# Performance work log

Hardware: AMD Instinct MI355X
Metric: run time of the kernel (lower is better)

Reference implementation:

```python
import jax, jax.numpy as jnp
import numpy as np

B, T, H = 4, 1024, 4096
N_Q, N_KV, HD = 32, 8, 128
N_REP = N_Q // N_KV
THETA = 10000.0


def setup_inputs() -> dict:
    key = jax.random.key(0)
    k0, k1, k2 = jax.random.split(key, 3)
    x = jax.random.normal(k0, (B, T, H), dtype=jnp.float32)
    w_qkv = jax.random.normal(k1, ((N_Q + 2 * N_KV) * HD, H), dtype=jnp.float32) * 0.02
    w_proj = jax.random.normal(k2, (N_Q * HD, H), dtype=jnp.float32).T * 0.02  # [H, N_Q*HD] -> stored as [out,in]=[4096,4096]
    # real RoPE frequencies, matching precompute_freqs_cis(theta=10000)
    inv_freq = 1.0 / (THETA ** (np.arange(0, HD, 2, dtype=np.float32) / HD))  # [HD/2]
    angles = np.arange(T, dtype=np.float32)[:, None] * inv_freq[None, :]      # [T, HD/2]
    freqs_cos = jnp.asarray(np.cos(angles))
    freqs_sin = jnp.asarray(np.sin(angles))
    return {"x": x, "w_qkv": w_qkv, "w_proj": w_proj,
            "freqs_cos": freqs_cos, "freqs_sin": freqs_sin}


def _rope(x, cos, sin):
    # x: [B, T, nH, HD]; consecutive pairs (x[2i], x[2i+1]) form complex numbers
    x0 = x[..., 0::2]
    x1 = x[..., 1::2]
    c = cos[None, :, None, :]
    s = sin[None, :, None, :]
    r0 = x0 * c - x1 * s
    r1 = x0 * s + x1 * c
    return jnp.stack([r0, r1], axis=-1).reshape(x.shape)


def reference(x, w_qkv, w_proj, freqs_cos, freqs_sin):
    q_per_kv = N_Q // N_KV
    qkv = jnp.einsum('bth,oh->bto', x, w_qkv)                 # [B,T,(N_Q+2*N_KV)*HD]
    qkv = qkv.reshape(B, T, N_KV, q_per_kv + 2, HD)           # interleaved GQA layout
    q = qkv[:, :, :, :q_per_kv, :].reshape(B, T, N_Q, HD)
    k = qkv[:, :, :, q_per_kv, :]                              # [B,T,N_KV,HD]
    v = qkv[:, :, :, q_per_kv + 1, :]
    q = _rope(q, freqs_cos, freqs_sin)
    k = _rope(k, freqs_cos, freqs_sin)
    k = jnp.repeat(k, N_REP, axis=2)                           # [B,T,N_Q,HD]
    v = jnp.repeat(v, N_REP, axis=2)
    q = q.transpose(0, 2, 1, 3)                                # [B,H,T,HD]
    k = k.transpose(0, 2, 1, 3)
    v = v.transpose(0, 2, 1, 3)
    scale = 1.0 / jnp.sqrt(jnp.float32(HD))
    scores = jnp.einsum('bhqd,bhkd->bhqk', q, k) * scale       # [B,H,T,T]
    causal = jnp.tril(jnp.ones((T, T), dtype=bool))
    scores = jnp.where(causal[None, None], scores, jnp.finfo(scores.dtype).min)
    attn = jax.nn.softmax(scores, axis=-1)
    out = jnp.einsum('bhqk,bhkd->bhqd', attn, v)               # [B,H,T,HD]
    out = out.transpose(0, 2, 1, 3).reshape(B, T, N_Q * HD)
    return jnp.einsum('bto,ho->bth', out, w_proj)              # RowParallel proj, [B,T,H]
```

## Files before the change

### kernel.cpp

```cpp
#include <hip/hip_runtime.h>
#include <cstddef>

#define DEVINL __device__ __forceinline__

typedef float f32x4 __attribute__((ext_vector_type(4)));
typedef __bf16 bf16x8 __attribute__((ext_vector_type(8)));

DEVINL unsigned short f2bf(float f) {
  union { float f; unsigned int u; } v; v.f = f;
  unsigned int u = v.u;
  unsigned int r = (u + 0x7fffu + ((u >> 16) & 1u)) >> 16;
  return (unsigned short)r;
}
DEVINL float bf2f(unsigned short s) {
  union { unsigned int u; float f; } v; v.u = ((unsigned int)s) << 16;
  return v.f;
}
DEVINL uint4 pack8(const unsigned short o[8]) {
  uint4 r;
  r.x = (unsigned int)o[0] | ((unsigned int)o[1] << 16);
  r.y = (unsigned int)o[2] | ((unsigned int)o[3] << 16);
  r.z = (unsigned int)o[4] | ((unsigned int)o[5] << 16);
  r.w = (unsigned int)o[6] | ((unsigned int)o[7] << 16);
  return r;
}
DEVINL void gload16(const void* g, void* l) {
  __builtin_amdgcn_global_load_lds(
      (__attribute__((address_space(1))) void*)g,
      (__attribute__((address_space(3))) void*)l, 16, 0, 0);
}

__global__ __launch_bounds__(256) void k_cvt(const float* __restrict__ in,
                                             unsigned short* __restrict__ out, int n4) {
  int i = blockIdx.x * 256 + threadIdx.x;
  if (i >= n4) return;
  float4 v = ((const float4*)in)[i];
  ushort4 o;
  o.x = f2bf(v.x); o.y = f2bf(v.y); o.z = f2bf(v.z); o.w = f2bf(v.w);
  ((ushort4*)out)[i] = o;
}

template <int OUT_BF16>
__global__ __launch_bounds__(512, 1) void k_gemm256(const unsigned short* __restrict__ A,
                                                    const unsigned short* __restrict__ Bt,
                                                    void* __restrict__ Cout,
                                                    int M, int N, int K) {
  __shared__ __align__(16) unsigned short As[2][2][256 * 32];
  __shared__ __align__(16) unsigned short Bs[2][2][256 * 32];
  const int t = threadIdx.x, lane = t & 63;
  const int wid = t >> 6, wm = wid >> 2, wn = wid & 3;
  const int fr = lane & 15, kq = lane >> 4;
  const int nwg = gridDim.x * gridDim.y;
  int lin = blockIdx.y * gridDim.x + blockIdx.x;
  lin = (lin & 7) * (nwg >> 3) + (lin >> 3);
  const int bx = lin % gridDim.x, by = lin / gridDim.x;
  const int row0 = by * 256, col0 = bx * 256;
  const int NT = K >> 6;

  int srow[2], sgs[2];
#pragma unroll
  for (int i = 0; i < 2; ++i) {
    const int off = (i * 512 + t) * 16;
    srow[i] = off >> 6;
    sgs[i] = (((off >> 4) & 3) - (srow[i] >> 1)) & 3;
  }

#define STAGE_A(KT, KS)                                                        \
  do {                                                                         \
    const int b_ = (KT) & 1;                                                   \
    _Pragma("unroll") for (int i = 0; i < 2; ++i)                              \
        gload16(A + (size_t)(row0 + srow[i]) * K + (KT) * 64 + (KS) * 32 +     \
                    sgs[i] * 8,                                                \
                (char*)&As[b_][KS][0] + i * 8192 + wid * 1024);                \
  } while (0)
#define STAGE_B(KT, KS)                                                        \
  do {                                                                         \
    const int b_ = (KT) & 1;                                                   \
    _Pragma("unroll") for (int i = 0; i < 2; ++i)                              \
        gload16(Bt + (size_t)(col0 + srow[i]) * K + (KT) * 64 + (KS) * 32 +    \
                    sgs[i] * 8,                                                \
                (char*)&Bs[b_][KS][0] + i * 8192 + wid * 1024);                \
  } while (0)
#define LDFRAG(BUFP, ROW) \
  (*(const bf16x8*)((const char*)(BUFP) + (ROW) * 64 + ((((ROW) >> 1) + kq & 3) << 4)))

  f32x4 acc[8][4];
#pragma unroll
  for (int m = 0; m < 8; ++m)
#pragma unroll
    for (int n = 0; n < 4; ++n) acc[m][n] = f32x4{0.f, 0.f, 0.f, 0.f};

  STAGE_A(0, 0); STAGE_B(0, 0); STAGE_A(0, 1); STAGE_B(0, 1);
  STAGE_A(1, 0); STAGE_B(1, 0);
  asm volatile("s_waitcnt vmcnt(4)" ::: "memory");
  __builtin_amdgcn_s_barrier();

  for (int kt = 0; kt < NT; ++kt) {
    const unsigned short* As0 = &As[kt & 1][0][0];
    const unsigned short* As1 = &As[kt & 1][1][0];
    const unsigned short* Bs0 = &Bs[kt & 1][0][0];
    const unsigned short* Bs1 = &Bs[kt & 1][1][0];
    bf16x8 a0[4], a1[4], b0[4], b1[4];

#pragma unroll
    for (int m = 0; m < 4; ++m) a0[m] = LDFRAG(As0, wm * 128 + m * 16 + fr);
#pragma unroll
    for (int n = 0; n < 4; ++n) b0[n] = LDFRAG(Bs0, wn * 64 + n * 16 + fr);
    if (kt + 1 < NT) STAGE_A(kt + 1, 1);
    __builtin_amdgcn_sched_barrier(0);
    __builtin_amdgcn_s_barrier();
    asm volatile("s_waitcnt lgkmcnt(0)" ::: "memory");
    __builtin_amdgcn_sched_barrier(0);
    __builtin_amdgcn_s_setprio(1);
#pragma unroll
    for (int m = 0; m < 4; ++m)
#pragma unroll
      for (int n = 0; n < 4; ++n)
        acc[m][n] = __builtin_amdgcn_mfma_f32_16x16x32_bf16(a0[m], b0[n], acc[m][n], 0, 0, 0);
    __builtin_amdgcn_s_setprio(0);
    __builtin_amdgcn_s_barrier();

#pragma unroll
    for (int m = 0; m < 4; ++m) a1[m] = LDFRAG(As0, wm * 128 + 64 + m * 16 + fr);
    if (kt + 1 < NT) STAGE_B(kt + 1, 1);
    __builtin_amdgcn_sched_barrier(0);
    __builtin_amdgcn_s_barrier();
    asm volatile("s_waitcnt lgkmcnt(0)" ::: "memory");
    __builtin_amdgcn_sched_barrier(0);
    __builtin_amdgcn_s_setprio(1);
#pragma unroll
    for (int m = 0; m < 4; ++m)
#pragma unroll
      for (int n = 0; n < 4; ++n)
        acc[m + 4][n] = __builtin_amdgcn_mfma_f32_16x16x32_bf16(a1[m], b0[n], acc[m + 4][n], 0, 0, 0);
    __builtin_amdgcn_s_setprio(0);
    __builtin_amdgcn_s_barrier();

#pragma unroll
    for (int m = 0; m < 4; ++m) a0[m] = LDFRAG(As1, wm * 128 + m * 16 + fr);
#pragma unroll
    for (int n = 0; n < 4; ++n) b1[n] = LDFRAG(Bs1, wn * 64 + n * 16 + fr);
    if (kt + 2 < NT) STAGE_A(kt + 2, 0);
    __builtin_amdgcn_sched_barrier(0);
    __builtin_amdgcn_s_barrier();
    asm volatile("s_waitcnt lgkmcnt(0)" ::: "memory");
    __builtin_amdgcn_sched_barrier(0);
    __builtin_amdgcn_s_setprio(1);
#pragma unroll
    for (int m = 0; m < 4; ++m)
#pragma unroll
      for (int n = 0; n < 4; ++n)
        acc[m][n] = __builtin_amdgcn_mfma_f32_16x16x32_bf16(a0[m], b1[n], acc[m][n], 0, 0, 0);
    __builtin_amdgcn_s_setprio(0);
    __builtin_amdgcn_s_barrier();

#pragma unroll
    for (int m = 0; m < 4; ++m) a1[m] = LDFRAG(As1, wm * 128 + 64 + m * 16 + fr);
    if (kt + 1 < NT) {
      if (kt + 2 < NT) asm volatile("s_waitcnt vmcnt(2)" ::: "memory");
      else             asm volatile("s_waitcnt vmcnt(0)" ::: "memory");
    }
    if (kt + 2 < NT) STAGE_B(kt + 2, 0);
    __builtin_amdgcn_sched_barrier(0);
    __builtin_amdgcn_s_barrier();
    asm volatile("s_waitcnt lgkmcnt(0)" ::: "memory");
    __builtin_amdgcn_sched_barrier(0);
    __builtin_amdgcn_s_setprio(1);
#pragma unroll
    for (int m = 0; m < 4; ++m)
#pragma unroll
      for (int n = 0; n < 4; ++n)
        acc[m + 4][n] = __builtin_amdgcn_mfma_f32_16x16x32_bf16(a1[m], b1[n], acc[m + 4][n], 0, 0, 0);
    __builtin_amdgcn_s_setprio(0);
    __builtin_amdgcn_s_barrier();
  }
#undef STAGE_A
#undef STAGE_B
#undef LDFRAG

  const int rsub = kq * 4;
#pragma unroll
  for (int m = 0; m < 8; ++m)
#pragma unroll
    for (int n = 0; n < 4; ++n)
#pragma unroll
      for (int r = 0; r < 4; ++r) {
        const size_t row = (size_t)row0 + wm * 128 + m * 16 + rsub + r;
        const size_t col = (size_t)col0 + wn * 64 + n * 16 + fr;
        if (OUT_BF16)
          ((unsigned short*)Cout)[row * N + col] = f2bf(acc[m][n][r]);
        else
          ((float*)Cout)[row * N + col] = acc[m][n][r];
      }
}

__global__ __launch_bounds__(256) void k_rope(const unsigned short* __restrict__ qkv,
                                              const float* __restrict__ fcos,
                                              const float* __restrict__ fsin,
                                              unsigned short* __restrict__ Qb,
                                              unsigned short* __restrict__ Kb) {
  const int idx = blockIdx.x * 256 + threadIdx.x;
  if (idx >= 4096 * 640) return;
  const int bt = idx / 640;
  const int r = idx - bt * 640;
  const int g = r / 80;
  const int rr = r - g * 80;
  const int slot = rr >> 4;
  const int d0 = (rr & 15) * 8;
  const int o0 = g * 768 + slot * 128 + d0;
  const int b = bt >> 10, tt = bt & 1023;

  uint4 raw = *(const uint4*)&qkv[(size_t)bt * 6144 + o0];
  unsigned short us[8] = {
      (unsigned short)(raw.x & 0xffff), (unsigned short)(raw.x >> 16),
      (unsigned short)(raw.y & 0xffff), (unsigned short)(raw.y >> 16),
      (unsigned short)(raw.z & 0xffff), (unsigned short)(raw.z >> 16),
      (unsigned short)(raw.w & 0xffff), (unsigned short)(raw.w >> 16)};

  float4 c = *(const float4*)&fcos[tt * 64 + (d0 >> 1)];
  float4 s = *(const float4*)&fsin[tt * 64 + (d0 >> 1)];
  const float sc = (slot < 4) ? 0.08838834764831845f : 1.0f;
  float cj[4] = {c.x, c.y, c.z, c.w};
  float sj[4] = {s.x, s.y, s.z, s.w};
  unsigned short os[8];
#pragma unroll
  for (int j = 0; j < 4; ++j) {
    float x0 = bf2f(us[2 * j]), x1 = bf2f(us[2 * j + 1]);
    os[2 * j] = f2bf((x0 * cj[j] - x1 * sj[j]) * sc);
    os[2 * j + 1] = f2bf((x0 * sj[j] + x1 * cj[j]) * sc);
  }
  if (slot < 4) {
    const int h = g * 4 + slot;
    *(uint4*)&Qb[((size_t)(b * 32 + h) * 1024 + tt) * 128 + d0] = pack8(os);
  } else {
    *(uint4*)&Kb[((size_t)(b * 8 + g) * 1024 + tt) * 128 + d0] = pack8(os);
  }
}

__global__ __launch_bounds__(256) void k_vtrans(const unsigned short* __restrict__ qkv,
                                                unsigned short* __restrict__ VT) {
  const int t = threadIdx.x;
  const int tt0 = blockIdx.x * 128;
  const int bg = blockIdx.y;
  const int b = bg >> 3, g = bg & 7;
  const int tj = t & 15;
  const int ti = t >> 4;
  union U4 { uint4 v; unsigned int u[4]; };
  U4 in[8], out[8];
  const unsigned short* src =
      qkv + (size_t)(b * 1024 + tt0 + ti * 8) * 6144 + g * 768 + 640 + tj * 8;
#pragma unroll
  for (int r = 0; r < 8; ++r) in[r].v = *(const uint4*)(src + (size_t)r * 6144);
#pragma unroll
  for (int c = 0; c < 8; ++c) {
    const unsigned int sel = (c & 1) ? 0x07060302u : 0x05040100u;
    const int dw = c >> 1;
#pragma unroll
    for (int w = 0; w < 4; ++w)
      out[c].u[w] = __builtin_amdgcn_perm(in[2 * w + 1].u[dw], in[2 * w].u[dw], sel);
  }
  unsigned short* dst = VT + (size_t)bg * 131072 + (size_t)(tj * 8) * 1024 + tt0 + ti * 8;
#pragma unroll
  for (int c = 0; c < 8; ++c) *(uint4*)(dst + (size_t)c * 1024) = out[c].v;
}

__global__ __launch_bounds__(512, 1) void k_attn(const unsigned short* __restrict__ Qb,
                                                 const unsigned short* __restrict__ Kb,
                                                 const unsigned short* __restrict__ VT,
                                                 unsigned short* __restrict__ AO) {
  __shared__ __align__(16) unsigned short Ks[2][64 * 128];
  __shared__ __align__(16) unsigned short Vt[2][128 * 64];
  __shared__ __align__(16) unsigned short Ps[8][32 * 64];
  const int t = threadIdx.x, lane = t & 63, wid = t >> 6;
  const int hh = wid >> 1, qh = wid & 1;
  const int bg = blockIdx.x, b = bg >> 3, g = bg & 7;
  const int qi = 15 - (int)blockIdx.y;
  const int q0 = qi * 64;
  const int h = g * 4 + hh;
  const int fr = lane & 15, kq = lane >> 4;
  const size_t kvbase = (size_t)bg * (1024 * 128);
  const size_t vtbase = (size_t)bg * (128 * 1024);

#define ASTAGE(TILE, BUF)                                                      \
  do {                                                                         \
    const int kv0_ = (TILE) * 64;                                              \
    _Pragma("unroll") for (int it = 0; it < 2; ++it) {                         \
      const int off = it * 8192 + t * 16;                                      \
      const int r_ = off >> 8, cb_ = off & 255;                                \
      const int scb_ = cb_ ^ ((r_ & 7) << 4);                                  \
      gload16(Kb + kvbase + (size_t)(kv0_ + r_) * 128 + (scb_ >> 1),           \
              (char*)Ks[BUF] + off);                                           \
    }                                                                          \
    _Pragma("unroll") for (int it = 0; it < 2; ++it) {                         \
      const int off = it * 8192 + t * 16;                                      \
      const int rd_ = off >> 7, cb_ = off & 127;                               \
      const int scb_ = cb_ ^ ((rd_ & 7) << 4);                                 \
      gload16(VT + vtbase + (size_t)rd_ * 1024 + kv0_ + (scb_ >> 1),           \
              (char*)Vt[BUF] + off);                                           \
    }                                                                          \
  } while (0)

  bf16x8 qf[2][4];
  {
    const unsigned short* Qp0 = Qb + ((size_t)(b * 32 + h) * 1024 + q0 + qh * 32) * 128;
#pragma unroll
    for (int qr = 0; qr < 2; ++qr)
#pragma unroll
      for (int ks = 0; ks < 4; ++ks)
        qf[qr][ks] = *(const bf16x8*)&Qp0[(size_t)(qr * 16 + fr) * 128 + ks * 32 + kq * 8];
  }
  float mrow[2][4], lrow[2][4];
#pragma unroll
  for (int qr = 0; qr < 2; ++qr)
#pragma unroll
    for (int rg = 0; rg < 4; ++rg) { mrow[qr][rg] = -1e30f; lrow[qr][rg] = 0.f; }
  f32x4 of[2][8];
#pragma unroll
  for (int qr = 0; qr < 2; ++qr)
#pragma unroll
    for (int n = 0; n < 8; ++n) of[qr][n] = f32x4{0.f, 0.f, 0.f, 0.f};

  const int ntiles = qi + 1;
  ASTAGE(0, 0);

  for (int kt = 0; kt < ntiles; ++kt) {
    const int buf = kt & 1;
    const int kv0 = kt * 64;
    if (kt + 1 < ntiles) {
      ASTAGE(kt + 1, buf ^ 1);
      asm volatile("s_waitcnt vmcnt(4)" ::: "memory");
    } else {
      asm volatile("s_waitcnt vmcnt(0)" ::: "memory");
    }
    __builtin_amdgcn_s_barrier();
    __builtin_amdgcn_sched_barrier(0);

    f32x4 sacc[2][4];
#pragma unroll
    for (int qr = 0; qr < 2; ++qr)
#pragma unroll
      for (int n = 0; n < 4; ++n) sacc[qr][n] = f32x4{0.f, 0.f, 0.f, 0.f};
#pragma unroll
    for (int n = 0; n < 4; ++n) {
      const int row = n * 16 + fr;
      const int sw = (row & 7) << 4;
      bf16x8 kf[4];
#pragma unroll
      for (int ks = 0; ks < 4; ++ks)
        kf[ks] = *(const bf16x8*)((const char*)Ks[buf] + row * 256 + ((ks * 64 + kq * 16) ^ sw));
      __builtin_amdgcn_s_setprio(1);
#pragma unroll
      for (int qr = 0; qr < 2; ++qr)
#pragma unroll
        for (int ks = 0; ks < 4; ++ks)
          sacc[qr][n] =
              __builtin_amdgcn_mfma_f32_16x16x32_bf16(qf[qr][ks], kf[ks], sacc[qr][n], 0, 0, 0);
      __builtin_amdgcn_s_setprio(0);
    }

#pragma unroll
    for (int qr = 0; qr < 2; ++qr)
#pragma unroll
      for (int rg = 0; rg < 4; ++rg) {
        const int qrow = q0 + qh * 32 + qr * 16 + kq * 4 + rg;
        float s[4];
#pragma unroll
        for (int n = 0; n < 4; ++n) {
          s[n] = sacc[qr][n][rg];
          if (kv0 + n * 16 + fr > qrow) s[n] = -1e30f;
        }
        float mx = fmaxf(fmaxf(s[0], s[1]), fmaxf(s[2], s[3]));
#pragma unroll
        for (int o = 1; o < 16; o <<= 1) mx = fmaxf(mx, __shfl_xor(mx, o));
        if (mx > mrow[qr][rg] + 8.f) {
          const float fac = __expf(mrow[qr][rg] - mx);
          lrow[qr][rg] *= fac;
#pragma unroll
          for (int n = 0; n < 8; ++n) of[qr][n][rg] *= fac;
          mrow[qr][rg] = mx;
        }
        const float mcur = mrow[qr][rg];
        float p[4];
#pragma unroll
        for (int n = 0; n < 4; ++n) p[n] = __expf(s[n] - mcur);
        float sum = (p[0] + p[1]) + (p[2] + p[3]);
#pragma unroll
        for (int o = 1; o < 16; o <<= 1) sum += __shfl_xor(sum, o);
        lrow[qr][rg] += sum;
        const int q = qr * 16 + kq * 4 + rg;
        const int swp = (q & 7) << 4;
#pragma unroll
        for (int n = 0; n < 4; ++n)
          *(unsigned short*)((char*)Ps[wid] + q * 128 + ((2 * (n * 16 + fr)) ^ swp)) =
              f2bf(p[n]);
      }
    asm volatile("s_waitcnt lgkmcnt(0)" ::: "memory");
    __builtin_amdgcn_sched_barrier(0);

    bf16x8 pa[2][2];
#pragma unroll
    for (int qr = 0; qr < 2; ++qr) {
      const int prow = qr * 16 + fr;
      const int swp = (prow & 7) << 4;
#pragma unroll
      for (int kk = 0; kk < 2; ++kk)
        pa[qr][kk] = *(const bf16x8*)((const char*)Ps[wid] + prow * 128 +
                                      ((kk * 64 + kq * 16) ^ swp));
    }
#pragma unroll
    for (int n = 0; n < 8; ++n) {
      const int row = n * 16 + fr;
      const int sw = (row & 7) << 4;
      bf16x8 vf[2];
#pragma unroll
      for (int kk = 0; kk < 2; ++kk)
        vf[kk] = *(const bf16x8*)((const char*)Vt[buf] + row * 128 + ((kk * 64 + kq * 16) ^ sw));
      __builtin_amdgcn_s_setprio(1);
#pragma unroll
      for (int qr = 0; qr < 2; ++qr)
#pragma unroll
        for (int kk = 0; kk < 2; ++kk)
          of[qr][n] = __builtin_amdgcn_mfma_f32_16x16x32_bf16(pa[qr][kk], vf[kk], of[qr][n], 0, 0, 0);
      __builtin_amdgcn_s_setprio(0);
    }
    asm volatile("s_waitcnt lgkmcnt(0)" ::: "memory");
    __builtin_amdgcn_sched_barrier(0);
    __builtin_amdgcn_s_barrier();
  }
#undef ASTAGE

  float inv[2][4];
#pragma unroll
  for (int qr = 0; qr < 2; ++qr)
#pragma unroll
    for (int rg = 0; rg < 4; ++rg) inv[qr][rg] = 1.0f / lrow[qr][rg];
#pragma unroll
  for (int qr = 0; qr < 2; ++qr)
#pragma unroll
    for (int n = 0; n < 8; ++n)
#pragma unroll
      for (int rg = 0; rg < 4; ++rg) {
        const size_t row = (size_t)b * 1024 + q0 + qh * 32 + qr * 16 + kq * 4 + rg;
        const size_t col = (size_t)h * 128 + n * 16 + fr;
        AO[row * 4096 + col] = f2bf(of[qr][n][rg] * inv[qr][rg]);
      }
}

extern "C" void kernel_launch(void* const* d_in, const int* in_sizes, int n_in,
                              void* d_out, int out_size, void* d_ws, size_t ws_size,
                              hipStream_t stream) {
  const float* x = (const float*)d_in[0];
  const float* w_qkv = (const float*)d_in[1];
  const float* w_proj = (const float*)d_in[2];
  const float* fcos = (const float*)d_in[3];
  const float* fsin = (const float*)d_in[4];
  float* out = (float*)d_out;

  char* ws = (char*)d_ws;
  unsigned short* XB    = (unsigned short*)(ws + 0);
  unsigned short* WQKVB = (unsigned short*)(ws + 33554432);
  unsigned short* QKVB  = (unsigned short*)(ws + 83886080);
  unsigned short* QB    = (unsigned short*)(ws + 134217728);
  unsigned short* KB    = (unsigned short*)(ws + 167772160);
  unsigned short* VTB   = (unsigned short*)(ws + 176160768);
  unsigned short* WPROJB = XB;
  unsigned short* AOB    = QKVB;

  k_cvt<<<16384, 256, 0, stream>>>(x, XB, 4194304);
  k_cvt<<<24576, 256, 0, stream>>>(w_qkv, WQKVB, 6291456);
  k_gemm256<1><<<dim3(24, 16), 512, 0, stream>>>(XB, WQKVB, QKVB, 4096, 6144, 4096);
  k_cvt<<<16384, 256, 0, stream>>>(w_proj, WPROJB, 4194304);
  k_rope<<<10240, 256, 0, stream>>>(QKVB, fcos, fsin, QB, KB);
  k_vtrans<<<dim3(8, 32), 256, 0, stream>>>(QKVB, VTB);
  k_attn<<<dim3(32, 16), 512, 0, stream>>>(QB, KB, VTB, AOB);
  k_gemm256<0><<<dim3(16, 16), 512, 0, stream>>>(AOB, WPROJB, out, 4096, 4096, 4096);
}
```

Before: 515.6 us.

## Switch GEMM to 32x32x16 MFMA tiles and merge conversion kernels

```diff
diff --git a/kernel.cpp b/kernel.cpp
--- a/kernel.cpp
+++ b/kernel.cpp
@@ -4,6 +4,7 @@
 #define DEVINL __device__ __forceinline__
 
 typedef float f32x4 __attribute__((ext_vector_type(4)));
+typedef float f32x16 __attribute__((ext_vector_type(16)));
 typedef __bf16 bf16x8 __attribute__((ext_vector_type(8)));
 
 DEVINL unsigned short f2bf(float f) {
@@ -30,10 +31,22 @@
       (__attribute__((address_space(3))) void*)l, 16, 0, 0);
 }
 
-__global__ __launch_bounds__(256) void k_cvt(const float* __restrict__ in,
-                                             unsigned short* __restrict__ out, int n4) {
+__global__ __launch_bounds__(256) void k_cvt_all(const float* __restrict__ x,
+                                                 const float* __restrict__ wq,
+                                                 const float* __restrict__ wp,
+                                                 unsigned short* __restrict__ xb,
+                                                 unsigned short* __restrict__ wqb,
+                                                 unsigned short* __restrict__ wpb) {
   int i = blockIdx.x * 256 + threadIdx.x;
-  if (i >= n4) return;
+  const float* in;
+  unsigned short* out;
+  if (i < 4194304) {
+    in = x; out = xb;
+  } else if (i < 4194304 + 6291456) {
+    in = wq; out = wqb; i -= 4194304;
+  } else {
+    in = wp; out = wpb; i -= 4194304 + 6291456;
+  }
   float4 v = ((const float4*)in)[i];
   ushort4 o;
   o.x = f2bf(v.x); o.y = f2bf(v.y); o.z = f2bf(v.z); o.w = f2bf(v.w);
@@ -49,7 +62,8 @@
   __shared__ __align__(16) unsigned short Bs[2][2][256 * 32];
   const int t = threadIdx.x, lane = t & 63;
   const int wid = t >> 6, wm = wid >> 2, wn = wid & 3;
-  const int fr = lane & 15, kq = lane >> 4;
+  const int lrow = lane & 31;
+  const int khalf = lane >> 5;
   const int nwg = gridDim.x * gridDim.y;
   int lin = blockIdx.y * gridDim.x + blockIdx.x;
   lin = (lin & 7) * (nwg >> 3) + (lin >> 3);
@@ -81,14 +95,17 @@
                     sgs[i] * 8,                                                \
                 (char*)&Bs[b_][KS][0] + i * 8192 + wid * 1024);                \
   } while (0)
-#define LDFRAG(BUFP, ROW) \
-  (*(const bf16x8*)((const char*)(BUFP) + (ROW) * 64 + ((((ROW) >> 1) + kq & 3) << 4)))
-
-  f32x4 acc[8][4];
-#pragma unroll
-  for (int m = 0; m < 8; ++m)
-#pragma unroll
-    for (int n = 0; n < 4; ++n) acc[m][n] = f32x4{0.f, 0.f, 0.f, 0.f};
+#define LDF32(BUFP, ROW, KK)                                                   \
+  (*(const bf16x8*)((const char*)(BUFP) + (ROW) * 64 +                         \
+                    ((((KK) * 2 + khalf + ((ROW) >> 1)) & 3) << 4)))
+
+  f32x16 acc[4][2];
+#pragma unroll
+  for (int m = 0; m < 4; ++m)
+#pragma unroll
+    for (int n = 0; n < 2; ++n)
+#pragma unroll
+      for (int r = 0; r < 16; ++r) acc[m][n][r] = 0.f;
 
   STAGE_A(0, 0); STAGE_B(0, 0); STAGE_A(0, 1); STAGE_B(0, 1);
   STAGE_A(1, 0); STAGE_B(1, 0);
@@ -100,12 +117,18 @@
     const unsigned short* As1 = &As[kt & 1][1][0];
     const unsigned short* Bs0 = &Bs[kt & 1][0][0];
     const unsigned short* Bs1 = &Bs[kt & 1][1][0];
-    bf16x8 a0[4], a1[4], b0[4], b1[4];
-
-#pragma unroll
-    for (int m = 0; m < 4; ++m) a0[m] = LDFRAG(As0, wm * 128 + m * 16 + fr);
-#pragma unroll
-    for (int n = 0; n < 4; ++n) b0[n] = LDFRAG(Bs0, wn * 64 + n * 16 + fr);
+    bf16x8 a[2][2], bfr[2][2];
+
+#pragma unroll
+    for (int m = 0; m < 2; ++m)
+#pragma unroll
+      for (int kk = 0; kk < 2; ++kk)
+        a[m][kk] = LDF32(As0, wm * 128 + m * 32 + lrow, kk);
+#pragma unroll
+    for (int n = 0; n < 2; ++n)
+#pragma unroll
+      for (int kk = 0; kk < 2; ++kk)
+        bfr[n][kk] = LDF32(Bs0, wn * 64 + n * 32 + lrow, kk);
     if (kt + 1 < NT) STAGE_A(kt + 1, 1);
     __builtin_amdgcn_sched_barrier(0);
     __builtin_amdgcn_s_barrier();
@@ -113,15 +136,21 @@
     __builtin_amdgcn_sched_barrier(0);
     __builtin_amdgcn_s_setprio(1);
 #pragma unroll
-    for (int m = 0; m < 4; ++m)
-#pragma unroll
-      for (int n = 0; n < 4; ++n)
-        acc[m][n] = __builtin_amdgcn_mfma_f32_16x16x32_bf16(a0[m], b0[n], acc[m][n], 0, 0, 0);
+    for (int m = 0; m < 2; ++m)
+#pragma unroll
+      for (int n = 0; n < 2; ++n)
+#pragma unroll
+        for (int kk = 0; kk < 2; ++kk)
+          acc[m][n] = __builtin_amdgcn_mfma_f32_32x32x16_bf16(a[m][kk], bfr[n][kk],
+                                                              acc[m][n], 0, 0, 0);
     __builtin_amdgcn_s_setprio(0);
     __builtin_amdgcn_s_barrier();
 
 #pragma unroll
-    for (int m = 0; m < 4; ++m) a1[m] = LDFRAG(As0, wm * 128 + 64 + m * 16 + fr);
+    for (int m = 0; m < 2; ++m)
+#pragma unroll
+      for (int kk = 0; kk < 2; ++kk)
+        a[m][kk] = LDF32(As0, wm * 128 + (m + 2) * 32 + lrow, kk);
     if (kt + 1 < NT) STAGE_B(kt + 1, 1);
     __builtin_amdgcn_sched_barrier(0);
     __builtin_amdgcn_s_barrier();
@@ -129,17 +158,26 @@
     __builtin_amdgcn_sched_barrier(0);
     __builtin_amdgcn_s_setprio(1);
 #pragma unroll
-    for (int m = 0; m < 4; ++m)
-#pragma unroll
-      for (int n = 0; n < 4; ++n)
-        acc[m + 4][n] = __builtin_amdgcn_mfma_f32_16x16x32_bf16(a1[m], b0[n], acc[m + 4][n], 0, 0, 0);
+    for (int m = 0; m < 2; ++m)
+#pragma unroll
+      for (int n = 0; n < 2; ++n)
+#pragma unroll
+        for (int kk = 0; kk < 2; ++kk)
+          acc[m + 2][n] = __builtin_amdgcn_mfma_f32_32x32x16_bf16(a[m][kk], bfr[n][kk],
+                                                                  acc[m + 2][n], 0, 0, 0);
     __builtin_amdgcn_s_setprio(0);
     __builtin_amdgcn_s_barrier();
 
 #pragma unroll
-    for (int m = 0; m < 4; ++m) a0[m] = LDFRAG(As1, wm * 128 + m * 16 + fr);
-#pragma unroll
-    for (int n = 0; n < 4; ++n) b1[n] = LDFRAG(Bs1, wn * 64 + n * 16 + fr);
+    for (int m = 0; m < 2; ++m)
+#pragma unroll
+      for (int kk = 0; kk < 2; ++kk)
+        a[m][kk] = LDF32(As1, wm * 128 + m * 32 + lrow, kk);
+#pragma unroll
+    for (int n = 0; n < 2; ++n)
+#pragma unroll
+      for (int kk = 0; kk < 2; ++kk)
+        bfr[n][kk] = LDF32(Bs1, wn * 64 + n * 32 + lrow, kk);
     if (kt + 2 < NT) STAGE_A(kt + 2, 0);
     __builtin_amdgcn_sched_barrier(0);
     __builtin_amdgcn_s_barrier();
@@ -147,15 +185,21 @@
     __builtin_amdgcn_sched_barrier(0);
     __builtin_amdgcn_s_setprio(1);
 #pragma unroll
-    for (int m = 0; m < 4; ++m)
-#pragma unroll
-      for (int n = 0; n < 4; ++n)
-        acc[m][n] = __builtin_amdgcn_mfma_f32_16x16x32_bf16(a0[m], b1[n], acc[m][n], 0, 0, 0);
+    for (int m = 0; m < 2; ++m)
+#pragma unroll
+      for (int n = 0; n < 2; ++n)
+#pragma unroll
+        for (int kk = 0; kk < 2; ++kk)
+          acc[m][n] = __builtin_amdgcn_mfma_f32_32x32x16_bf16(a[m][kk], bfr[n][kk],
+                                                              acc[m][n], 0, 0, 0);
     __builtin_amdgcn_s_setprio(0);
     __builtin_amdgcn_s_barrier();
 
 #pragma unroll
-    for (int m = 0; m < 4; ++m) a1[m] = LDFRAG(As1, wm * 128 + 64 + m * 16 + fr);
+    for (int m = 0; m < 2; ++m)
+#pragma unroll
+      for (int kk = 0; kk < 2; ++kk)
+        a[m][kk] = LDF32(As1, wm * 128 + (m + 2) * 32 + lrow, kk);
     if (kt + 1 < NT) {
       if (kt + 2 < NT) asm volatile("s_waitcnt vmcnt(2)" ::: "memory");
       else             asm volatile("s_waitcnt vmcnt(0)" ::: "memory");
@@ -167,26 +211,29 @@
     __builtin_amdgcn_sched_barrier(0);
     __builtin_amdgcn_s_setprio(1);
 #pragma unroll
-    for (int m = 0; m < 4; ++m)
-#pragma unroll
-      for (int n = 0; n < 4; ++n)
-        acc[m + 4][n] = __builtin_amdgcn_mfma_f32_16x16x32_bf16(a1[m], b1[n], acc[m + 4][n], 0, 0, 0);
+    for (int m = 0; m < 2; ++m)
+#pragma unroll
+      for (int n = 0; n < 2; ++n)
+#pragma unroll
+        for (int kk = 0; kk < 2; ++kk)
+          acc[m + 2][n] = __builtin_amdgcn_mfma_f32_32x32x16_bf16(a[m][kk], bfr[n][kk],
+                                                                  acc[m + 2][n], 0, 0, 0);
     __builtin_amdgcn_s_setprio(0);
     __builtin_amdgcn_s_barrier();
   }
 #undef STAGE_A
 #undef STAGE_B
-#undef LDFRAG
-
-  const int rsub = kq * 4;
-#pragma unroll
-  for (int m = 0; m < 8; ++m)
-#pragma unroll
-    for (int n = 0; n < 4; ++n)
-#pragma unroll
-      for (int r = 0; r < 4; ++r) {
-        const size_t row = (size_t)row0 + wm * 128 + m * 16 + rsub + r;
-        const size_t col = (size_t)col0 + wn * 64 + n * 16 + fr;
+#undef LDF32
+
+#pragma unroll
+  for (int m = 0; m < 4; ++m)
+#pragma unroll
+    for (int n = 0; n < 2; ++n)
+#pragma unroll
+      for (int r = 0; r < 16; ++r) {
+        const size_t row = (size_t)row0 + wm * 128 + m * 32 +
+                           (r & 3) + 8 * (r >> 2) + 4 * khalf;
+        const size_t col = (size_t)col0 + wn * 64 + n * 32 + lrow;
         if (OUT_BF16)
           ((unsigned short*)Cout)[row * N + col] = f2bf(acc[m][n][r]);
         else
@@ -463,13 +510,11 @@
   unsigned short* QB    = (unsigned short*)(ws + 134217728);
   unsigned short* KB    = (unsigned short*)(ws + 167772160);
   unsigned short* VTB   = (unsigned short*)(ws + 176160768);
-  unsigned short* WPROJB = XB;
+  unsigned short* WPROJB = (unsigned short*)(ws + 184549376);
   unsigned short* AOB    = QKVB;
 
-  k_cvt<<<16384, 256, 0, stream>>>(x, XB, 4194304);
-  k_cvt<<<24576, 256, 0, stream>>>(w_qkv, WQKVB, 6291456);
+  k_cvt_all<<<57344, 256, 0, stream>>>(x, w_qkv, w_proj, XB, WQKVB, WPROJB);
   k_gemm256<1><<<dim3(24, 16), 512, 0, stream>>>(XB, WQKVB, QKVB, 4096, 6144, 4096);
-  k_cvt<<<16384, 256, 0, stream>>>(w_proj, WPROJB, 4194304);
   k_rope<<<10240, 256, 0, stream>>>(QKVB, fcos, fsin, QB, KB);
   k_vtrans<<<dim3(8, 32), 256, 0, stream>>>(QKVB, VTB);
   k_attn<<<dim3(32, 16), 512, 0, stream>>>(QB, KB, VTB, AOB);
```

Result: slower. 545.3 us (+5.7%).
